# Kernel tuning notes

Measured on AMD Instinct MI355X. Metric: run time of the kernel, lower is better.

Reference implementation:

```python
import jax, jax.numpy as jnp
import numpy as np


def setup_inputs() -> dict:
    key = jax.random.key(0)
    k1, k2 = jax.random.split(key)
    B, D, H, W = 32, 256, 32, 32
    K = 1024
    z = jax.random.normal(k1, (B, D, H, W), dtype=jnp.float32)
    # torch init is uniform(-1/K, 1/K); randn scaled keeps same scale class
    embedding_weight = jax.random.uniform(k2, (K, D), dtype=jnp.float32,
                                          minval=-1.0 / K, maxval=1.0 / K)
    return {"z": z, "embedding_weight": embedding_weight}


def reference(z, embedding_weight):
    # z: [B, D, H, W] -> [B, H, W, D]
    z_nhwc = jnp.transpose(z, (0, 2, 3, 1))
    B, H, W, D = z_nhwc.shape
    z_flat = z_nhwc.reshape(-1, D)                      # [N, D]
    # squared distances: ||z||^2 + ||e||^2 - 2 z @ e^T   -> [N, K]
    d = (jnp.sum(z_flat ** 2, axis=1, keepdims=True)
         + jnp.sum(embedding_weight ** 2, axis=1)
         - 2.0 * z_flat @ embedding_weight.T)
    min_encoding_indices = jnp.argmin(d, axis=1)        # [N] int
    z_q = embedding_weight[min_encoding_indices].reshape(B, H, W, D)
    memodecode_loss = (jax.lax.stop_gradient(z_q) - z_nhwc) ** 2  # [B,H,W,D]
    z_q_out = jnp.transpose(z_q, (0, 3, 1, 2))          # [B, D, H, W]
    return (z_q_out, min_encoding_indices, memodecode_loss)
```

## Files before the change

### kernel.cpp

```cpp
#include <hip/hip_runtime.h>

#define DD 256
#define HWN 1024
#define NN 32768
#define KK 1024
#define MARGIN 1e-4f
#define FLAGBIT (1 << 30)

#define ZQ_OFF   0
#define IDX_OFF  8388608
#define LOSS_OFF 8421376

#define WS_NEED 38146112

typedef __attribute__((ext_vector_type(8))) _Float16 f16x8;
typedef __attribute__((ext_vector_type(4))) float f32x4;
typedef unsigned long long u64;

__device__ __forceinline__ ushort f2h(float x) {
    _Float16 h = (_Float16)x;
    return *reinterpret_cast<ushort*>(&h);
}
__device__ __forceinline__ float h2f(ushort u) {
    _Float16 h = *reinterpret_cast<_Float16*>(&u);
    return (float)h;
}

__device__ __forceinline__ int swz(int r, int kgi) {
    return (r << 2) + (kgi ^ (r & 3) ^ ((r >> 2) & 3));
}

__global__ __launch_bounds__(64) void k_e2(const float* __restrict__ E,
                                           float* __restrict__ e2) {
    int k = (blockIdx.x << 6) + threadIdx.x;
    const float* row = E + (size_t)k * DD;
    float half_[2];
#pragma unroll
    for (int h = 0; h < 2; ++h) {
        const float* a = row + (h << 7);
        float r[8];
#pragma unroll
        for (int j = 0; j < 8; ++j) r[j] = __fmul_rn(a[j], a[j]);
        for (int i = 8; i < 128; i += 8) {
#pragma unroll
            for (int j = 0; j < 8; ++j) {
                float x = a[i + j];
                r[j] = __fadd_rn(r[j], __fmul_rn(x, x));
            }
        }
        half_[h] = __fadd_rn(__fadd_rn(__fadd_rn(r[0], r[1]), __fadd_rn(r[2], r[3])),
                             __fadd_rn(__fadd_rn(r[4], r[5]), __fadd_rn(r[6], r[7])));
    }
    e2[k] = __fadd_rn(half_[0], half_[1]);
}

__global__ __launch_bounds__(256) void k_prepZ2(const float* __restrict__ Z,
                                                ushort* __restrict__ Zh,
                                                float* __restrict__ z2) {
    __shared__ float zc[32][257];
    const int g = blockIdx.x;
    const int b = g >> 5;
    const int hw0 = (g & 31) << 5;
    const int th = threadIdx.x;
    const int n0 = (b << 10) + hw0;

#pragma unroll
    for (int j = 0; j < 32; ++j) {
        int li = (j << 8) + th;
        int d = li >> 5;
        int hl = li & 31;
        zc[hl][d] = Z[(size_t)((b << 8) + d) * HWN + hw0 + hl];
    }
    __syncthreads();

    {
        int r = th >> 3, c = th & 7;
        ushort hs[32];
#pragma unroll
        for (int i = 0; i < 32; ++i) hs[i] = f2h(zc[r][(c << 5) + i]);
        size_t addr = (size_t)(n0 + r) * DD + (c << 5);
#pragma unroll
        for (int q = 0; q < 4; ++q)
            *reinterpret_cast<f16x8*>(&Zh[addr + (q << 3)]) =
                *reinterpret_cast<f16x8*>(&hs[q << 3]);
    }

    {
        const int row = th >> 3, j = th & 7;
        const float* a = &zc[row][0];
        float x0 = a[j];
        float r0 = __fmul_rn(x0, x0);
        float x1 = a[128 + j];
        float r1 = __fmul_rn(x1, x1);
#pragma unroll
        for (int i = 8; i < 128; i += 8) {
            float y0 = a[i + j];
            r0 = __fadd_rn(r0, __fmul_rn(y0, y0));
            float y1 = a[128 + i + j];
            r1 = __fadd_rn(r1, __fmul_rn(y1, y1));
        }
#pragma unroll
        for (int m = 1; m <= 4; m <<= 1) {
            r0 = __fadd_rn(r0, __shfl_xor(r0, m));
            r1 = __fadd_rn(r1, __shfl_xor(r1, m));
        }
        if (j == 0) z2[n0 + row] = __fadd_rn(r0, r1);
    }
}

__global__ __launch_bounds__(256) void k_z2(const float* __restrict__ Z,
                                            float* __restrict__ z2) {
    int n = (blockIdx.x << 8) + threadIdx.x;
    int b = n >> 10, hw = n & 1023;
    const float* base = Z + (size_t)(b << 8) * HWN + hw;
    float half_[2];
#pragma unroll
    for (int h = 0; h < 2; ++h) {
        const float* a = base + (size_t)(h << 7) * HWN;
        float r[8];
#pragma unroll
        for (int j = 0; j < 8; ++j) {
            float x = a[(size_t)j * HWN];
            r[j] = __fmul_rn(x, x);
        }
        for (int i = 8; i < 128; i += 8) {
#pragma unroll
            for (int j = 0; j < 8; ++j) {
                float x = a[(size_t)(i + j) * HWN];
                r[j] = __fadd_rn(r[j], __fmul_rn(x, x));
            }
        }
        half_[h] = __fadd_rn(__fadd_rn(__fadd_rn(r[0], r[1]), __fadd_rn(r[2], r[3])),
                             __fadd_rn(__fadd_rn(r[4], r[5]), __fadd_rn(r[6], r[7])));
    }
    z2[n] = __fadd_rn(half_[0], half_[1]);
}

__global__ __launch_bounds__(256) void k_prepE(const float* __restrict__ E,
                                               ushort* __restrict__ Eh,
                                               int* __restrict__ flagCount) {
    if (blockIdx.x == 0 && threadIdx.x == 0) *flagCount = 0;
    int i4 = (blockIdx.x << 8) + threadIdx.x;
    float4 v = *reinterpret_cast<const float4*>(&E[(size_t)i4 << 2]);
    v.x *= 1024.f; v.y *= 1024.f; v.z *= 1024.f; v.w *= 1024.f;
    ushort4 h;
    h.x = f2h(v.x); h.y = f2h(v.y); h.z = f2h(v.z); h.w = f2h(v.w);
    *reinterpret_cast<ushort4*>(&Eh[(size_t)i4 << 2]) = h;
}

__device__ __forceinline__ void stage_kc(const ushort* __restrict__ Zh,
                                         const ushort* __restrict__ Eh,
                                         ushort* ldsbuf, int n0, int c0, int kc,
                                         int wid, int lane) {
#pragma unroll
    for (int is = 0; is < 4; ++is) {
        const int chunk = (wid << 2) + is;
        const int arr = chunk >> 3;
        const int cb8 = chunk & 7;
        const int s = (cb8 << 6) + lane;
        const int r = s >> 2;
        const int kgi = (s & 3) ^ (r & 3) ^ ((r >> 2) & 3);
        const ushort* g = (arr == 0) ? Zh + (size_t)(n0 + r) * DD
                                     : Eh + (size_t)(c0 + r) * DD;
        g += (kc << 5) + (kgi << 3);
        ushort* l = ldsbuf + arr * 4096 + (cb8 << 9);
        __builtin_amdgcn_global_load_lds(
            (const __attribute__((address_space(1))) void*)g,
            (__attribute__((address_space(3))) void*)l, 16, 0, 0);
    }
}

__global__ __launch_bounds__(256) void k_dist_mfma(const ushort* __restrict__ Zh,
                                                   const ushort* __restrict__ Eh,
                                                   const float* __restrict__ e2,
                                                   float* __restrict__ part) {
    __shared__ ushort lds[2][2][4096];
    float (*red)[2][3] = reinterpret_cast<float (*)[2][3]>(&lds[0][0][0]);

    const int B = blockIdx.x;
    const int xcd = B & 7;
    const int j = B >> 3;
    const int cb = j & 7;
    const int rb = (xcd << 5) + (j >> 3);
    const int n0 = rb << 7, c0 = cb << 7;
    const int th = threadIdx.x;
    const int wid = th >> 6, lane = th & 63;
    const int wr = wid >> 1, wc = wid & 1;
    const int fr = lane & 15, kgi = lane >> 4;

    f32x4 acc[4][4];
#pragma unroll
    for (int i = 0; i < 4; ++i)
#pragma unroll
        for (int jj = 0; jj < 4; ++jj) acc[i][jj] = (f32x4){0.f, 0.f, 0.f, 0.f};

    int zoff[4], eoff[4];
#pragma unroll
    for (int mi = 0; mi < 4; ++mi)
        zoff[mi] = swz((wr << 6) + (mi << 4) + fr, kgi) << 4;
#pragma unroll
    for (int ni = 0; ni < 4; ++ni)
        eoff[ni] = swz((wc << 6) + (ni << 4) + fr, kgi) << 4;

    stage_kc(Zh, Eh, &lds[0][0][0], n0, c0, 0, wid, lane);

    for (int kc = 0; kc < 8; ++kc) {
        __builtin_amdgcn_s_barrier();
        if (kc < 7) {
            stage_kc(Zh, Eh, &lds[(kc + 1) & 1][0][0], n0, c0, kc + 1, wid, lane);
            asm volatile("s_waitcnt vmcnt(4)" ::: "memory");
        } else {
            asm volatile("s_waitcnt vmcnt(0)" ::: "memory");
        }
        __builtin_amdgcn_s_barrier();

        const char* zb  = (const char*)&lds[kc & 1][0][0];
        const char* ebh = (const char*)&lds[kc & 1][1][0];
        f16x8 za[4], ea[4];
#pragma unroll
        for (int mi = 0; mi < 4; ++mi)
            za[mi] = *reinterpret_cast<const f16x8*>(zb + zoff[mi]);
#pragma unroll
        for (int ni = 0; ni < 4; ++ni)
            ea[ni] = *reinterpret_cast<const f16x8*>(ebh + eoff[ni]);
        __builtin_amdgcn_s_setprio(1);
#pragma unroll
        for (int mi = 0; mi < 4; ++mi)
#pragma unroll
            for (int ni = 0; ni < 4; ++ni)
                acc[mi][ni] = __builtin_amdgcn_mfma_f32_16x16x32_f16(za[mi], ea[ni], acc[mi][ni], 0, 0, 0);
        __builtin_amdgcn_s_setprio(0);
    }

    __syncthreads();

    float e2v[4];
#pragma unroll
    for (int ni = 0; ni < 4; ++ni) e2v[ni] = e2[c0 + (wc << 6) + (ni << 4) + fr];

#pragma unroll
    for (int mi = 0; mi < 4; ++mi) {
#pragma unroll
        for (int jj = 0; jj < 4; ++jj) {
            float m1 = __builtin_inff(), m2 = __builtin_inff(), bi = 3.4e38f;
#pragma unroll
            for (int ni = 0; ni < 4; ++ni) {
                float s = fmaf(-0x1p-9f, acc[mi][ni][jj], e2v[ni]);
                float c = (float)(c0 + (wc << 6) + (ni << 4) + fr);
                if (s < m1)      { m2 = m1; m1 = s; bi = c; }
                else if (s < m2) { m2 = s; }
            }
#pragma unroll
            for (int m = 1; m <= 8; m <<= 1) {
                float om1 = __shfl_xor(m1, m);
                float om2 = __shfl_xor(m2, m);
                float obi = __shfl_xor(bi, m);
                if (om1 < m1)       { m2 = fminf(m1, om2); m1 = om1; bi = obi; }
                else if (om1 == m1) { bi = fminf(bi, obi); m2 = m1; }
                else                { m2 = fminf(m2, om1); }
            }
            if (fr == 0) {
                int row = (wr << 6) + (mi << 4) + (kgi << 2) + jj;
                red[row][wc][0] = m1; red[row][wc][1] = m2; red[row][wc][2] = bi;
            }
        }
    }
    __syncthreads();
    if (th < 128) {
        float M1 = red[th][0][0], M2 = red[th][0][1], I = red[th][0][2];
        float v1 = red[th][1][0], v2 = red[th][1][1], vi = red[th][1][2];
        if (v1 < M1)       { M2 = fminf(M1, v2); M1 = v1; I = vi; }
        else if (v1 == M1) { I = fminf(I, vi); M2 = M1; }
        else               { M2 = fminf(M2, v1); }
        size_t p = ((size_t)(n0 + th) * 8 + cb) * 3;
        part[p] = M1; part[p + 1] = M2; part[p + 2] = I;
    }
}

__global__ __launch_bounds__(256) void k_combine(const float* __restrict__ part,
                                                 int* __restrict__ bestIdx,
                                                 int* __restrict__ flagList,
                                                 int* __restrict__ flagCount,
                                                 u64* __restrict__ bestG) {
    int n = (blockIdx.x << 8) + threadIdx.x;
    const float* p = part + (size_t)n * 24;
    float M1 = __builtin_inff(), M2 = __builtin_inff(), I = 3.4e38f;
    for (int c = 0; c < 8; ++c) {
        float v1 = p[c * 3], v2 = p[c * 3 + 1], vi = p[c * 3 + 2];
        if (v1 < M1)       { M2 = fminf(M1, v2); M1 = v1; I = vi; }
        else if (v1 == M1) { I = fminf(I, vi); M2 = M1; }
        else               { M2 = fminf(M2, v1); }
    }
    bestIdx[n] = (int)I;
    if (M2 - M1 < MARGIN) {
        bestG[n] = ~0ull;
        int pos = atomicAdd(flagCount, 1);
        flagList[pos] = n;
    }
}

__global__ __launch_bounds__(256) void k_refine4(const float* __restrict__ Z,
                                                 const float* __restrict__ E,
                                                 const float* __restrict__ e2,
                                                 const float* __restrict__ z2,
                                                 const int* __restrict__ flagList,
                                                 const int* __restrict__ flagCount,
                                                 u64* __restrict__ bestG) {
    __shared__ float zsh[DD];
    __shared__ float gbv[16];
    __shared__ int gbi[16];
    const int th = threadIdx.x;
    const int g = th >> 4;
    const int l = th & 15;
    const int cnt4 = (*flagCount) << 2;

    for (int jj = blockIdx.x; jj < cnt4; jj += (int)gridDim.x) {
        const int n = flagList[jj >> 2];
        const int q = jj & 3;
        const int b = n >> 10, hw = n & 1023;
        __syncthreads();
        if (th < DD) zsh[th] = Z[(size_t)((b << 8) + th) * HWN + hw];
        __syncthreads();
        float zr[16];
#pragma unroll
        for (int jq = 0; jq < 16; ++jq) zr[jq] = zsh[(l << 4) + jq];
        const float z2v = z2[n];
        float gbest = __builtin_inff();
        int bi = 0;

        const int base = q << 8;
        for (int it = 0; it < 4; ++it) {
            double dots[4];
#pragma unroll
            for (int u = 0; u < 4; ++u) {
                const int c = base + (it << 6) + (u << 4) + g;
                const float* er = &E[(size_t)c * DD + (l << 4)];
                float4 a0 = *reinterpret_cast<const float4*>(er);
                float4 a1 = *reinterpret_cast<const float4*>(er + 4);
                float4 a2 = *reinterpret_cast<const float4*>(er + 8);
                float4 a3 = *reinterpret_cast<const float4*>(er + 12);
                double s0 = (double)a0.x * zr[0]  + (double)a0.y * zr[1]
                          + (double)a0.z * zr[2]  + (double)a0.w * zr[3];
                double s1 = (double)a1.x * zr[4]  + (double)a1.y * zr[5]
                          + (double)a1.z * zr[6]  + (double)a1.w * zr[7];
                double s2 = (double)a2.x * zr[8]  + (double)a2.y * zr[9]
                          + (double)a2.z * zr[10] + (double)a2.w * zr[11];
                double s3 = (double)a3.x * zr[12] + (double)a3.y * zr[13]
                          + (double)a3.z * zr[14] + (double)a3.w * zr[15];
                dots[u] = (s0 + s1) + (s2 + s3);
            }
#pragma unroll
            for (int m = 1; m <= 8; m <<= 1) {
#pragma unroll
                for (int u = 0; u < 4; ++u)
                    dots[u] += __shfl_xor(dots[u], m);
            }
            if (l == 0) {
#pragma unroll
                for (int u = 0; u < 4; ++u) {
                    const int c = base + (it << 6) + (u << 4) + g;
                    float cc = (float)dots[u];
                    float t2 = __fmul_rn(2.0f, cc);
                    float gg = __fsub_rn(__fadd_rn(z2v, e2[c]), t2);
                    if (gg < gbest) { gbest = gg; bi = c; }
                }
            }
        }
        if (l == 0) { gbv[g] = gbest; gbi[g] = bi; }
        __syncthreads();
        if (th == 0) {
            float best = gbv[0]; int bbi = gbi[0];
            for (int qq = 1; qq < 16; ++qq) {
                float v = gbv[qq]; int vi = gbi[qq];
                if (v < best || (v == best && vi < bbi)) { best = v; bbi = vi; }
            }
            u64 pack = ((u64)__float_as_uint(best) << 32) | (unsigned)bbi;
            atomicMin(&bestG[n], pack);
        }
    }
}

__global__ __launch_bounds__(256) void k_final(const int* __restrict__ flagList,
                                               const int* __restrict__ flagCount,
                                               const u64* __restrict__ bestG,
                                               int* __restrict__ bestIdx) {
    const int cnt = *flagCount;
    for (int j = (blockIdx.x << 8) + threadIdx.x; j < cnt; j += (int)(gridDim.x << 8)) {
        int n = flagList[j];
        bestIdx[n] = (int)(unsigned)(bestG[n] & 0xFFFFFFFFull);
    }
}

#define UPD(m1, m2, i1, s, k)                            \
    do {                                                 \
        if ((s) < (m1)) { m2 = m1; m1 = (s); i1 = (k); } \
        else if ((s) < (m2)) { m2 = (s); }               \
    } while (0)

#define FMAJ(j, EV, C)                                   \
    acc[0][j] = fmaf(z4.x, EV.C, acc[0][j]);             \
    acc[1][j] = fmaf(z4.y, EV.C, acc[1][j]);             \
    acc[2][j] = fmaf(z4.z, EV.C, acc[2][j]);             \
    acc[3][j] = fmaf(z4.w, EV.C, acc[3][j]);

#define UROUND(u, C)                                                          \
    {                                                                         \
        float4 z4 = *reinterpret_cast<const float4*>(&zs[dq + u][ty4]);       \
        FMAJ(0, e0, C) FMAJ(1, e1, C) FMAJ(2, e2v, C) FMAJ(3, e3, C)          \
        FMAJ(4, e4, C) FMAJ(5, e5, C) FMAJ(6, e6, C) FMAJ(7, e7, C)           \
    }

__global__ __launch_bounds__(256, 3) void k_dist_f32(const float* __restrict__ Z,
                                                     const float* __restrict__ E,
                                                     const float* __restrict__ e2,
                                                     int* __restrict__ bestIdx) {
    __shared__ float zs[64][68];
    __shared__ float es[128][68];
    const int th = threadIdx.x;
    const int n0 = blockIdx.x << 6;
    const int b = n0 >> 10;
    const int hw0 = n0 & 1023;
    const int tx = th & 15;
    const int ty = th >> 4;
    const int ty4 = ty << 2;
    float m1[4], m2[4];
    int idx[4];
#pragma unroll
    for (int i = 0; i < 4; ++i) { m1[i] = __builtin_inff(); m2[i] = __builtin_inff(); idx[i] = 0; }
    for (int ct = 0; ct < 8; ++ct) {
        float acc[4][8];
#pragma unroll
        for (int i = 0; i < 4; ++i)
#pragma unroll
            for (int j = 0; j < 8; ++j) acc[i][j] = 0.f;
        for (int dc = 0; dc < 4; ++dc) {
            __syncthreads();
#pragma unroll
            for (int j = 0; j < 4; ++j) {
                int i4 = (j << 8) + th;
                int dd = i4 >> 4;
                int rr = (i4 & 15) << 2;
                *reinterpret_cast<float4*>(&zs[dd][rr]) =
                    *reinterpret_cast<const float4*>(
                        &Z[(size_t)((b << 8) + (dc << 6) + dd) * HWN + hw0 + rr]);
            }
#pragma unroll
            for (int j = 0; j < 8; ++j) {
                int i4 = (j << 8) + th;
                int c = i4 >> 4;
                int d4 = (i4 & 15) << 2;
                *reinterpret_cast<float4*>(&es[c][d4]) =
                    *reinterpret_cast<const float4*>(
                        &E[(size_t)((ct << 7) + c) * DD + (dc << 6) + d4]);
            }
            __syncthreads();
#pragma unroll
            for (int dq = 0; dq < 64; dq += 4) {
                float4 e0 = *reinterpret_cast<const float4*>(&es[tx][dq]);
                float4 e1 = *reinterpret_cast<const float4*>(&es[tx + 16][dq]);
                float4 e2v = *reinterpret_cast<const float4*>(&es[tx + 32][dq]);
                float4 e3 = *reinterpret_cast<const float4*>(&es[tx + 48][dq]);
                float4 e4 = *reinterpret_cast<const float4*>(&es[tx + 64][dq]);
                float4 e5 = *reinterpret_cast<const float4*>(&es[tx + 80][dq]);
                float4 e6 = *reinterpret_cast<const float4*>(&es[tx + 96][dq]);
                float4 e7 = *reinterpret_cast<const float4*>(&es[tx + 112][dq]);
                UROUND(0, x)
                UROUND(1, y)
                UROUND(2, z)
                UROUND(3, w)
            }
        }
#pragma unroll
        for (int j = 0; j < 8; ++j) {
            int c = (ct << 7) + tx + (j << 4);
            float en = e2[c];
#pragma unroll
            for (int i = 0; i < 4; ++i) {
                float s = fmaf(-2.f, acc[i][j], en);
                UPD(m1[i], m2[i], idx[i], s, c);
            }
        }
    }
    __syncthreads();
    float* red = &es[0][0];
#pragma unroll
    for (int i = 0; i < 4; ++i) {
        int r = ty4 + i;
        int base = ((r << 4) + tx) * 3;
        red[base] = m1[i]; red[base + 1] = m2[i]; red[base + 2] = (float)idx[i];
    }
    __syncthreads();
    if (th < 64) {
        float M1 = __builtin_inff(), M2 = __builtin_inff(), I = 3.4e38f;
        for (int t = 0; t < 16; ++t) {
            int base = ((th << 4) + t) * 3;
            float v1 = red[base], v2 = red[base + 1], vi = red[base + 2];
            if (v1 < M1)       { M2 = fminf(M1, v2); M1 = v1; I = vi; }
            else if (v1 == M1) { I = fminf(I, vi); M2 = fminf(M2, v1); M2 = fminf(M2, v2); }
            else               { M2 = fminf(M2, v1); }
        }
        int id = (int)I;
        bestIdx[n0 + th] = (M2 - M1 < MARGIN) ? (id | FLAGBIT) : id;
    }
}

__global__ __launch_bounds__(64) void k_refine(const float* __restrict__ Z,
                                               const float* __restrict__ E,
                                               const float* __restrict__ e2,
                                               const float* __restrict__ z2,
                                               int* __restrict__ bestIdx) {
    __shared__ float zr[DD];
    const int l = threadIdx.x;
    for (int i = 0; i < 16; ++i) {
        int n = (blockIdx.x << 4) + i;
        if (!(bestIdx[n] & FLAGBIT)) continue;
        int b = n >> 10, hw = n & 1023;
        __syncthreads();
#pragma unroll
        for (int j = 0; j < 4; ++j)
            zr[(l << 2) + j] = Z[(size_t)((b << 8) + (l << 2) + j) * HWN + hw];
        __syncthreads();
        const float z2v = z2[n];
        float gbest = __builtin_inff();
        int bi = KK;
        for (int kk = 0; kk < 16; ++kk) {
            int k = (kk << 6) + l;
            double dot = 0.0;
            for (int d = 0; d < DD; d += 4) {
                float4 e4 = *reinterpret_cast<const float4*>(&E[(size_t)k * DD + d]);
                dot += (double)e4.x * zr[d]     + (double)e4.y * zr[d + 1]
                     + (double)e4.z * zr[d + 2] + (double)e4.w * zr[d + 3];
            }
            float c = (float)dot;
            float t = __fmul_rn(2.0f, c);
            float gg = __fsub_rn(__fadd_rn(z2v, e2[k]), t);
            if (gg < gbest) { gbest = gg; bi = k; }
        }
#pragma unroll
        for (int off = 32; off > 0; off >>= 1) {
            float og = __shfl_down(gbest, off);
            int oi = __shfl_down(bi, off);
            if (og < gbest || (og == gbest && oi < bi)) { gbest = og; bi = oi; }
        }
        if (l == 0) bestIdx[n] = bi;
    }
}

__global__ __launch_bounds__(256) void k_out(const ushort* __restrict__ Zh,
                                             const float* __restrict__ E,
                                             const int* __restrict__ bestIdx,
                                             float* __restrict__ out) {
    __shared__ int idxs[64];
    const int th = threadIdx.x;
    const int n0 = blockIdx.x << 6;
    const int b = n0 >> 10;
    const int hw0 = n0 & 1023;

    if (th < 64) {
        int id = bestIdx[n0 + th] & 1023;
        idxs[th] = id;
        out[IDX_OFF + n0 + th] = (float)id;
    }
    __syncthreads();

#pragma unroll
    for (int j = 0; j < 16; ++j) {
        int i4 = (j << 8) + th;
        int r = i4 >> 6;
        int f = (i4 & 63) << 2;
        int n = n0 + r;
        float4 e4 = *reinterpret_cast<const float4*>(&E[(size_t)idxs[r] * DD + f]);
        ushort4 zu = *reinterpret_cast<const ushort4*>(&Zh[(size_t)n * DD + f]);
        float4 o;
        float t;
        t = e4.x - h2f(zu.x); o.x = t * t;
        t = e4.y - h2f(zu.y); o.y = t * t;
        t = e4.z - h2f(zu.z); o.z = t * t;
        t = e4.w - h2f(zu.w); o.w = t * t;
        *reinterpret_cast<float4*>(&out[LOSS_OFF + (size_t)n * DD + f]) = o;
    }

#pragma unroll
    for (int dc = 0; dc < 4; ++dc)
#pragma unroll
        for (int j = 0; j < 16; ++j) {
            int li = (j << 8) + th;
            int dd = li >> 6;
            int r = li & 63;
            out[ZQ_OFF + (size_t)((b << 8) + (dc << 6) + dd) * HWN + hw0 + r] =
                E[(size_t)idxs[r] * DD + (dc << 6) + dd];
        }
}

__global__ __launch_bounds__(256) void k_out_f32(const float* __restrict__ Z,
                                                 const float* __restrict__ E,
                                                 const int* __restrict__ bestIdx,
                                                 float* __restrict__ out) {
    __shared__ float zc[64][68];
    __shared__ int idxs[64];
    const int th = threadIdx.x;
    const int n0 = blockIdx.x << 6;
    const int b = n0 >> 10;
    const int hw0 = n0 & 1023;

    if (th < 64) {
        int id = bestIdx[n0 + th] & 1023;
        idxs[th] = id;
        out[IDX_OFF + n0 + th] = (float)id;
    }
    __syncthreads();

    for (int dc = 0; dc < 4; ++dc) {
        __syncthreads();
#pragma unroll
        for (int j = 0; j < 16; ++j) {
            int li = (j << 8) + th;
            int dd = li >> 6;
            int r = li & 63;
            zc[r][dd] = Z[(size_t)((b << 8) + (dc << 6) + dd) * HWN + hw0 + r];
        }
        __syncthreads();
#pragma unroll
        for (int j = 0; j < 4; ++j) {
            int i4 = (j << 8) + th;
            int r = i4 >> 4;
            int f = (i4 & 15) << 2;
            float4 e4 = *reinterpret_cast<const float4*>(
                &E[(size_t)idxs[r] * DD + (dc << 6) + f]);
            float4 z4 = *reinterpret_cast<const float4*>(&zc[r][f]);
            float4 o;
            o.x = (e4.x - z4.x) * (e4.x - z4.x);
            o.y = (e4.y - z4.y) * (e4.y - z4.y);
            o.z = (e4.z - z4.z) * (e4.z - z4.z);
            o.w = (e4.w - z4.w) * (e4.w - z4.w);
            *reinterpret_cast<float4*>(
                &out[LOSS_OFF + (size_t)(n0 + r) * DD + (dc << 6) + f]) = o;
        }
#pragma unroll
        for (int j = 0; j < 16; ++j) {
            int li = (j << 8) + th;
            int dd = li >> 6;
            int r = li & 63;
            out[ZQ_OFF + (size_t)((b << 8) + (dc << 6) + dd) * HWN + hw0 + r] =
                E[(size_t)idxs[r] * DD + (dc << 6) + dd];
        }
    }
}

extern "C" void kernel_launch(void* const* d_in, const int* in_sizes, int n_in,
                              void* d_out, int out_size, void* d_ws, size_t ws_size,
                              hipStream_t stream) {
    const float* Z = (const float*)d_in[0];
    const float* E = (const float*)d_in[1];
    float* out = (float*)d_out;
    char* ws = (char*)d_ws;
    float* e2 = (float*)ws;
    float* z2 = (float*)(ws + 4096);
    int* bestIdx = (int*)(ws + 135168);

    k_e2<<<KK / 64, 64, 0, stream>>>(E, e2);

    if (ws_size >= WS_NEED) {
        float* part = (float*)(ws + 266240);
        ushort* Eh = (ushort*)(ws + 3411968);
        ushort* Zh = (ushort*)(ws + 4460544);
        u64* bestG = (u64*)(ws + 21237760);
        int* flagCount = (int*)(ws + 38014976);
        int* flagList = (int*)(ws + 38015040);
        k_prepE<<<256, 256, 0, stream>>>(E, Eh, flagCount);
        k_prepZ2<<<1024, 256, 0, stream>>>(Z, Zh, z2);
        k_dist_mfma<<<2048, 256, 0, stream>>>(Zh, Eh, e2, part);
        k_combine<<<NN / 256, 256, 0, stream>>>(part, bestIdx, flagList, flagCount, bestG);
        k_refine4<<<4096, 256, 0, stream>>>(Z, E, e2, z2, flagList, flagCount, bestG);
        k_final<<<64, 256, 0, stream>>>(flagList, flagCount, bestG, bestIdx);
        k_out<<<NN / 64, 256, 0, stream>>>(Zh, E, bestIdx, out);
    } else {
        k_z2<<<NN / 256, 256, 0, stream>>>(Z, z2);
        k_dist_f32<<<NN / 64, 256, 0, stream>>>(Z, E, e2, bestIdx);
        k_refine<<<NN / 16, 64, 0, stream>>>(Z, E, e2, z2, bestIdx);
        k_out_f32<<<NN / 64, 256, 0, stream>>>(Z, E, bestIdx, out);
    }
}
```

Baseline: 158.5 us.

## Batch four flagged rows per refine block, parallelize e2, stage z_q gather in LDS

The refine kernel now handles four flagged rows per work item, so each codebook row loaded from global memory is reused across four double-precision dot products instead of one, and the grid is halved. The e2 kernel splits each row across 8 lanes with shuffle reductions, using 256-thread blocks for more parallelism. The output kernel stages gathered codebook rows in a padded LDS tile before the transposed z_q write, replacing scattered strided global reads. The e2 summation order changes, which could alter ties slightly, and the refine kernel pads partial groups by duplicating the last flagged row.

```diff
diff --git a/kernel.cpp b/kernel.cpp
--- a/kernel.cpp
+++ b/kernel.cpp
@@ -30,28 +30,29 @@
     return (r << 2) + (kgi ^ (r & 3) ^ ((r >> 2) & 3));
 }
 
-__global__ __launch_bounds__(64) void k_e2(const float* __restrict__ E,
-                                           float* __restrict__ e2) {
-    int k = (blockIdx.x << 6) + threadIdx.x;
-    const float* row = E + (size_t)k * DD;
-    float half_[2];
-#pragma unroll
-    for (int h = 0; h < 2; ++h) {
-        const float* a = row + (h << 7);
-        float r[8];
-#pragma unroll
-        for (int j = 0; j < 8; ++j) r[j] = __fmul_rn(a[j], a[j]);
-        for (int i = 8; i < 128; i += 8) {
-#pragma unroll
-            for (int j = 0; j < 8; ++j) {
-                float x = a[i + j];
-                r[j] = __fadd_rn(r[j], __fmul_rn(x, x));
-            }
-        }
-        half_[h] = __fadd_rn(__fadd_rn(__fadd_rn(r[0], r[1]), __fadd_rn(r[2], r[3])),
-                             __fadd_rn(__fadd_rn(r[4], r[5]), __fadd_rn(r[6], r[7])));
-    }
-    e2[k] = __fadd_rn(half_[0], half_[1]);
+__global__ __launch_bounds__(256) void k_e2(const float* __restrict__ E,
+                                            float* __restrict__ e2) {
+    const int th = threadIdx.x;
+    const int row = (blockIdx.x << 5) + (th >> 3);
+    const int j = th & 7;
+    const float* a = E + (size_t)row * DD;
+    float x0 = a[j];
+    float r0 = __fmul_rn(x0, x0);
+    float x1 = a[128 + j];
+    float r1 = __fmul_rn(x1, x1);
+#pragma unroll
+    for (int i = 8; i < 128; i += 8) {
+        float y0 = a[i + j];
+        r0 = __fadd_rn(r0, __fmul_rn(y0, y0));
+        float y1 = a[128 + i + j];
+        r1 = __fadd_rn(r1, __fmul_rn(y1, y1));
+    }
+#pragma unroll
+    for (int m = 1; m <= 4; m <<= 1) {
+        r0 = __fadd_rn(r0, __shfl_xor(r0, m));
+        r1 = __fadd_rn(r1, __shfl_xor(r1, m));
+    }
+    if (j == 0) e2[row] = __fadd_rn(r0, r1);
 }
 
 __global__ __launch_bounds__(256) void k_prepZ2(const float* __restrict__ Z,
@@ -299,38 +300,54 @@
     }
 }
 
-__global__ __launch_bounds__(256) void k_refine4(const float* __restrict__ Z,
+__global__ __launch_bounds__(256) void k_refine5(const float* __restrict__ Z,
                                                  const float* __restrict__ E,
                                                  const float* __restrict__ e2,
                                                  const float* __restrict__ z2,
                                                  const int* __restrict__ flagList,
                                                  const int* __restrict__ flagCount,
                                                  u64* __restrict__ bestG) {
-    __shared__ float zsh[DD];
-    __shared__ float gbv[16];
-    __shared__ int gbi[16];
+    __shared__ float zsh[4][DD];
+    __shared__ float gbv[16][4];
+    __shared__ int gbi[16][4];
+    __shared__ int rown[4];
     const int th = threadIdx.x;
     const int g = th >> 4;
     const int l = th & 15;
-    const int cnt4 = (*flagCount) << 2;
-
-    for (int jj = blockIdx.x; jj < cnt4; jj += (int)gridDim.x) {
-        const int n = flagList[jj >> 2];
+    const int cnt = *flagCount;
+    const int items = ((cnt + 3) >> 2) << 2;
+
+    for (int jj = blockIdx.x; jj < items; jj += (int)gridDim.x) {
+        const int gi = jj >> 2;
         const int q = jj & 3;
-        const int b = n >> 10, hw = n & 1023;
-        __syncthreads();
-        if (th < DD) zsh[th] = Z[(size_t)((b << 8) + th) * HWN + hw];
-        __syncthreads();
-        float zr[16];
-#pragma unroll
-        for (int jq = 0; jq < 16; ++jq) zr[jq] = zsh[(l << 4) + jq];
-        const float z2v = z2[n];
-        float gbest = __builtin_inff();
-        int bi = 0;
+        __syncthreads();
+        if (th < 4) {
+            int fi = (gi << 2) + th;
+            if (fi >= cnt) fi = cnt - 1;
+            rown[th] = flagList[fi];
+        }
+        __syncthreads();
+#pragma unroll
+        for (int r = 0; r < 4; ++r) {
+            int n = rown[r];
+            zsh[r][th] = Z[(size_t)(((n >> 10) << 8) + th) * HWN + (n & 1023)];
+        }
+        __syncthreads();
+        float zr[4][16];
+#pragma unroll
+        for (int r = 0; r < 4; ++r)
+#pragma unroll
+            for (int jq = 0; jq < 16; ++jq) zr[r][jq] = zsh[r][(l << 4) + jq];
+        float z2v[4];
+#pragma unroll
+        for (int r = 0; r < 4; ++r) z2v[r] = z2[rown[r]];
+        float gbest[4];
+        int bi[4];
+#pragma unroll
+        for (int r = 0; r < 4; ++r) { gbest[r] = __builtin_inff(); bi[r] = 0; }
 
         const int base = q << 8;
         for (int it = 0; it < 4; ++it) {
-            double dots[4];
 #pragma unroll
             for (int u = 0; u < 4; ++u) {
                 const int c = base + (it << 6) + (u << 4) + g;
@@ -339,43 +356,50 @@
                 float4 a1 = *reinterpret_cast<const float4*>(er + 4);
                 float4 a2 = *reinterpret_cast<const float4*>(er + 8);
                 float4 a3 = *reinterpret_cast<const float4*>(er + 12);
-                double s0 = (double)a0.x * zr[0]  + (double)a0.y * zr[1]
-                          + (double)a0.z * zr[2]  + (double)a0.w * zr[3];
-                double s1 = (double)a1.x * zr[4]  + (double)a1.y * zr[5]
-                          + (double)a1.z * zr[6]  + (double)a1.w * zr[7];
-                double s2 = (double)a2.x * zr[8]  + (double)a2.y * zr[9]
-                          + (double)a2.z * zr[10] + (double)a2.w * zr[11];
-                double s3 = (double)a3.x * zr[12] + (double)a3.y * zr[13]
-                          + (double)a3.z * zr[14] + (double)a3.w * zr[15];
-                dots[u] = (s0 + s1) + (s2 + s3);
-            }
-#pragma unroll
-            for (int m = 1; m <= 8; m <<= 1) {
-#pragma unroll
-                for (int u = 0; u < 4; ++u)
-                    dots[u] += __shfl_xor(dots[u], m);
-            }
-            if (l == 0) {
-#pragma unroll
-                for (int u = 0; u < 4; ++u) {
-                    const int c = base + (it << 6) + (u << 4) + g;
-                    float cc = (float)dots[u];
-                    float t2 = __fmul_rn(2.0f, cc);
-                    float gg = __fsub_rn(__fadd_rn(z2v, e2[c]), t2);
-                    if (gg < gbest) { gbest = gg; bi = c; }
+                double dots[4];
+#pragma unroll
+                for (int r = 0; r < 4; ++r) {
+                    double s0 = (double)a0.x * zr[r][0]  + (double)a0.y * zr[r][1]
+                              + (double)a0.z * zr[r][2]  + (double)a0.w * zr[r][3];
+                    double s1 = (double)a1.x * zr[r][4]  + (double)a1.y * zr[r][5]
+                              + (double)a1.z * zr[r][6]  + (double)a1.w * zr[r][7];
+                    double s2 = (double)a2.x * zr[r][8]  + (double)a2.y * zr[r][9]
+                              + (double)a2.z * zr[r][10] + (double)a2.w * zr[r][11];
+                    double s3 = (double)a3.x * zr[r][12] + (double)a3.y * zr[r][13]
+                              + (double)a3.z * zr[r][14] + (double)a3.w * zr[r][15];
+                    dots[r] = (s0 + s1) + (s2 + s3);
                 }
-            }
-        }
-        if (l == 0) { gbv[g] = gbest; gbi[g] = bi; }
-        __syncthreads();
-        if (th == 0) {
-            float best = gbv[0]; int bbi = gbi[0];
+#pragma unroll
+                for (int m = 1; m <= 8; m <<= 1) {
+#pragma unroll
+                    for (int r = 0; r < 4; ++r)
+                        dots[r] += __shfl_xor(dots[r], m);
+                }
+                if (l == 0) {
+#pragma unroll
+                    for (int r = 0; r < 4; ++r) {
+                        float cc = (float)dots[r];
+                        float t2 = __fmul_rn(2.0f, cc);
+                        float gg = __fsub_rn(__fadd_rn(z2v[r], e2[c]), t2);
+                        if (gg < gbest[r]) { gbest[r] = gg; bi[r] = c; }
+                    }
+                }
+            }
+        }
+        if (l == 0) {
+#pragma unroll
+            for (int r = 0; r < 4; ++r) { gbv[g][r] = gbest[r]; gbi[g][r] = bi[r]; }
+        }
+        __syncthreads();
+        if (th < 4) {
+            const int r = th;
+            float best = gbv[0][r]; int bbi = gbi[0][r];
             for (int qq = 1; qq < 16; ++qq) {
-                float v = gbv[qq]; int vi = gbi[qq];
+                float v = gbv[qq][r]; int vi = gbi[qq][r];
                 if (v < best || (v == best && vi < bbi)) { best = v; bbi = vi; }
             }
             u64 pack = ((u64)__float_as_uint(best) << 32) | (unsigned)bbi;
-            atomicMin(&bestG[n], pack);
+            atomicMin(&bestG[rown[r]], pack);
         }
     }
 }
@@ -551,6 +575,7 @@
                                              const int* __restrict__ bestIdx,
                                              float* __restrict__ out) {
     __shared__ int idxs[64];
+    __shared__ float es[64][68];
     const int th = threadIdx.x;
     const int n0 = blockIdx.x << 6;
     const int b = n0 >> 10;
@@ -580,16 +605,26 @@
         *reinterpret_cast<float4*>(&out[LOSS_OFF + (size_t)n * DD + f]) = o;
     }
 
-#pragma unroll
-    for (int dc = 0; dc < 4; ++dc)
+    for (int dc = 0; dc < 4; ++dc) {
+        __syncthreads();
+        {
+            const int r = th >> 2, qd = (th & 3) << 4;
+            const float* er = &E[(size_t)idxs[r] * DD + (dc << 6) + qd];
+#pragma unroll
+            for (int v = 0; v < 4; ++v)
+                *reinterpret_cast<float4*>(&es[r][qd + (v << 2)]) =
+                    *reinterpret_cast<const float4*>(er + (v << 2));
+        }
+        __syncthreads();
 #pragma unroll
         for (int j = 0; j < 16; ++j) {
             int li = (j << 8) + th;
             int dd = li >> 6;
             int r = li & 63;
             out[ZQ_OFF + (size_t)((b << 8) + (dc << 6) + dd) * HWN + hw0 + r] =
-                E[(size_t)idxs[r] * DD + (dc << 6) + dd];
-        }
+                es[r][dd];
+        }
+    }
 }
 
 __global__ __launch_bounds__(256) void k_out_f32(const float* __restrict__ Z,
@@ -658,7 +693,7 @@
     float* z2 = (float*)(ws + 4096);
     int* bestIdx = (int*)(ws + 135168);
 
-    k_e2<<<KK / 64, 64, 0, stream>>>(E, e2);
+    k_e2<<<32, 256, 0, stream>>>(E, e2);
 
     if (ws_size >= WS_NEED) {
         float* part = (float*)(ws + 266240);
@@ -671,7 +706,7 @@
         k_prepZ2<<<1024, 256, 0, stream>>>(Z, Zh, z2);
         k_dist_mfma<<<2048, 256, 0, stream>>>(Zh, Eh, e2, part);
         k_combine<<<NN / 256, 256, 0, stream>>>(part, bestIdx, flagList, flagCount, bestG);
-        k_refine4<<<4096, 256, 0, stream>>>(Z, E, e2, z2, flagList, flagCount, bestG);
+        k_refine5<<<2048, 256, 0, stream>>>(Z, E, e2, z2, flagList, flagCount, bestG);
         k_final<<<64, 256, 0, stream>>>(flagList, flagCount, bestG, bestIdx);
         k_out<<<NN / 64, 256, 0, stream>>>(Zh, E, bestIdx, out);
     } else {
```

New measurement: 137.7 us (median of 2 runs). 13.1% less time.
